# Optimization experiments

Measured on AMD Instinct MI355X. Metric: run time of the kernel, lower is better.

## Reference

```python
import jax, jax.numpy as jnp
import numpy as np

B, T, D = 1, 4096, 1024
H, KD, VD = 16, 64, 64
MIN_THETA, MAX_THETA = 1.0, 10000.0


def setup_inputs() -> dict:
    key = jax.random.key(0)
    k0, k1, k2 = jax.random.split(key, 3)
    x = jax.random.normal(k0, (B, T, D), dtype=jnp.float32)
    W_in = jax.random.normal(k1, ((2 * KD + VD) * H, D), dtype=jnp.float32) * 0.02
    b_in = jnp.zeros(((2 * KD + VD) * H,), dtype=jnp.float32)
    W_out = jax.random.normal(k2, (D, H * VD), dtype=jnp.float32) * 0.02
    b_out = jnp.zeros((D,), dtype=jnp.float32)
    return {"x": x, "W_in": W_in, "b_in": b_in, "W_out": W_out, "b_out": b_out}


def _sin_cos(t, d, dtype):
    # geometric sequence of thetas over half the head dim
    half = d // 2
    p = jnp.arange(half, dtype=dtype) / (half - 1)
    thetas = MIN_THETA * (MAX_THETA / MIN_THETA) ** p  # [half]
    pos = jnp.arange(t, dtype=dtype)[:, None] / thetas[None, :]  # [T, half]
    return jnp.sin(pos), jnp.cos(pos)


def _rope(x, sin, cos):
    d = x.shape[-1] // 2
    x_hi, x_lo = x[..., :d], x[..., d:]
    y_lo = x_lo * cos + x_hi * sin
    y_hi = x_hi * cos - x_lo * sin
    return jnp.concatenate([y_lo, y_hi], axis=-1)


def reference(x, W_in, b_in, W_out, b_out):
    b, t, _ = x.shape
    proj = x @ W_in.T + b_in  # [B, T, (2KD+VD)*H]
    i1, i2 = KD * H, 2 * KD * H
    q = proj[..., :i1].reshape(b, t, H, KD).transpose(0, 2, 1, 3)   # [B,H,T,KD]
    k = proj[..., i1:i2].reshape(b, t, H, KD).transpose(0, 2, 1, 3)
    v = proj[..., i2:].reshape(b, t, H, VD).transpose(0, 2, 1, 3)   # [B,H,T,VD]
    sin, cos = _sin_cos(t, KD, x.dtype)
    q = _rope(q, sin, cos)
    k = _rope(k, sin, cos)
    scale = 1.0 / np.sqrt(KD)
    att = jnp.einsum('bhqd,bhkd->bhqk', q, k) * jnp.asarray(scale, x.dtype)
    mask = jnp.tril(jnp.ones((t, t), dtype=bool))  # causal
    att = jnp.where(mask[None, None], att, jnp.asarray(-jnp.inf, x.dtype))
    att = jax.nn.softmax(att, axis=-1)
    y = jnp.einsum('bhqk,bhkd->bhqd', att, v)
    y = y.transpose(0, 2, 1, 3).reshape(b, t, H * VD)
    return y @ W_out.T + b_out
```

## Files before the change

kernel.cpp:

```cpp
#include <hip/hip_runtime.h>
#include <math.h>

#define T_SEQ 4096
#define DMODEL 1024
#define NH 16
#define HD 64
#define NQT (T_SEQ / 64)

typedef _Float16 f16x4 __attribute__((ext_vector_type(4)));
typedef _Float16 f16x8 __attribute__((ext_vector_type(8)));
typedef float f32x4 __attribute__((ext_vector_type(4)));

#define HTD ((size_t)NH * T_SEQ * HD)

__global__ __launch_bounds__(256)
void sincos_table_kernel(float* __restrict__ tab) {
    int idx = blockIdx.x * 256 + threadIdx.x;
    if (idx >= T_SEQ * 32) return;
    int t = idx >> 5, j = idx & 31;
    double p = (double)((float)j / 31.0f);
    float theta = (float)pow(10000.0, p);
    float ang = (float)t / theta;
    double a = (double)ang;
    tab[t * 64 + j]      = (float)sin(a);
    tab[t * 64 + 32 + j] = (float)cos(a);
}

__global__ __launch_bounds__(256)
void cast3_kernel(const float* __restrict__ x, const float* __restrict__ wi,
                  const float* __restrict__ wo, _Float16* __restrict__ x16,
                  _Float16* __restrict__ wi16, _Float16* __restrict__ wo16) {
    size_t gid = (size_t)blockIdx.x * 256 + threadIdx.x;
    const float* src; _Float16* dst; size_t i;
    if (gid < 524288)       { src = x;  dst = x16;  i = gid; }
    else if (gid < 917504)  { src = wi; dst = wi16; i = gid - 524288; }
    else                    { src = wo; dst = wo16; i = gid - 917504; }
    float4 a = *((const float4*)src + i * 2);
    float4 b = *((const float4*)src + i * 2 + 1);
    f16x8 o = {(_Float16)a.x, (_Float16)a.y, (_Float16)a.z, (_Float16)a.w,
               (_Float16)b.x, (_Float16)b.y, (_Float16)b.z, (_Float16)b.w};
    *((f16x8*)dst + i) = o;
}

__global__ __launch_bounds__(256)
void rope16_kernel(_Float16* __restrict__ q16, _Float16* __restrict__ k16,
                   const float* __restrict__ tab) {
    int idx = blockIdx.x * 256 + threadIdx.x;
    int j = idx & 31;
    int t = (idx >> 5) & (T_SEQ - 1);
    int h = (idx >> 17) & (NH - 1);
    int z = idx >> 21;
    float s = tab[t * 64 + j];
    float c = tab[t * 64 + 32 + j];
    _Float16* base = (z ? k16 : q16) + ((size_t)h * T_SEQ + t) * HD;
    float a = (float)base[j], b = (float)base[j + 32];
    float lo = b * c + a * s;
    float hi = a * c - b * s;
    if (z == 0) { lo *= 0.125f; hi *= 0.125f; }
    base[j]      = (_Float16)lo;
    base[j + 32] = (_Float16)hi;
}

template<int EPI>
__global__ __launch_bounds__(256)
void gemm16_kernel(const _Float16* __restrict__ A, const _Float16* __restrict__ B,
                   const float* __restrict__ bias, float* __restrict__ out,
                   _Float16* __restrict__ outv, int M, int N, int K, int gx) {
    __shared__ _Float16 Alds[128 * 64];
    __shared__ _Float16 Blds[128 * 64];
    const int tid = threadIdx.x;
    const int w = tid >> 6, lane = tid & 63, lq = lane & 15, lg = lane >> 4;
    const int wr = w >> 1, wc = w & 1;

    int cpx = (int)gridDim.x >> 3;
    int tileid = (blockIdx.x & 7) * cpx + (blockIdx.x >> 3);
    const int bx = tileid % gx, by = tileid / gx;
    const int row0 = by * 128, col0 = bx * 128;

    const int ra = tid >> 1, ha = tid & 1;
    const _Float16* Ap = A + (size_t)(row0 + ra) * K + ha * 32;
    const _Float16* Bp = B + (size_t)(col0 + ra) * K + ha * 32;
    char* Awr = (char*)Alds + ra * 128;
    char* Bwr = (char*)Blds + ra * 128;
    int wsw[4];
#pragma unroll
    for (int j = 0; j < 4; ++j) wsw[j] = ((ha * 4 + j) ^ (ra & 7)) * 16;

    f32x4 acc[4][4] = {};
    f16x8 sa[4], sb[4];
#pragma unroll
    for (int j = 0; j < 4; ++j) {
        sa[j] = *(const f16x8*)(Ap + j * 8);
        sb[j] = *(const f16x8*)(Bp + j * 8);
    }

    const int nkt = K >> 6;
    for (int kt = 0; kt < nkt; ++kt) {
        __syncthreads();
#pragma unroll
        for (int j = 0; j < 4; ++j) {
            *(f16x8*)(Awr + wsw[j]) = sa[j];
            *(f16x8*)(Bwr + wsw[j]) = sb[j];
        }
        __syncthreads();
        if (kt + 1 < nkt) {
            int kn = (kt + 1) << 6;
#pragma unroll
            for (int j = 0; j < 4; ++j) {
                sa[j] = *(const f16x8*)(Ap + kn + j * 8);
                sb[j] = *(const f16x8*)(Bp + kn + j * 8);
            }
        }
#pragma unroll
        for (int ks = 0; ks < 2; ++ks) {
            f16x8 af[4], bf[4];
            const int cofs = ((ks * 4 + lg) ^ (lq & 7)) * 16;
#pragma unroll
            for (int i = 0; i < 4; ++i) {
                int rA = wr * 64 + i * 16 + lq;
                int rB = wc * 64 + i * 16 + lq;
                af[i] = *(const f16x8*)((char*)Alds + rA * 128 + cofs);
                bf[i] = *(const f16x8*)((char*)Blds + rB * 128 + cofs);
            }
#pragma unroll
            for (int mi = 0; mi < 4; ++mi)
#pragma unroll
                for (int nj = 0; nj < 4; ++nj)
                    acc[mi][nj] = __builtin_amdgcn_mfma_f32_16x16x32_f16(
                        af[mi], bf[nj], acc[mi][nj], 0, 0, 0);
        }
    }

    if (EPI == 0) {
#pragma unroll
        for (int nj = 0; nj < 4; ++nj) {
            int n = col0 + wc * 64 + nj * 16 + lq;
            float bv = bias[n];
#pragma unroll
            for (int mi = 0; mi < 4; ++mi) {
                int t0 = row0 + wr * 64 + mi * 16 + lg * 4;
#pragma unroll
                for (int r = 0; r < 4; ++r)
                    out[(size_t)(t0 + r) * N + n] = acc[mi][nj][r] + bv;
            }
        }
    } else {
        const int tensor = col0 >> 10;
        const int m0b = row0 + wr * 64;
        if (tensor == 2) {
#pragma unroll
            for (int nj = 0; nj < 4; ++nj) {
                int n = col0 + wc * 64 + nj * 16 + lq;
                int nn = n & 1023; int hh = nn >> 6, d = nn & 63;
                float bv = bias[n];
                _Float16* dv = outv + 2 * HTD + (size_t)(hh * 64 + d) * T_SEQ;
#pragma unroll
                for (int mi = 0; mi < 4; ++mi) {
                    int t0 = m0b + mi * 16 + lg * 4;
                    f16x4 val = {(_Float16)(acc[mi][nj][0] + bv),
                                 (_Float16)(acc[mi][nj][1] + bv),
                                 (_Float16)(acc[mi][nj][2] + bv),
                                 (_Float16)(acc[mi][nj][3] + bv)};
                    *(f16x4*)(dv + t0) = val;
                }
            }
        } else {
            _Float16* dst = outv + (size_t)tensor * HTD;
#pragma unroll
            for (int nj = 0; nj < 4; ++nj) {
                int n = col0 + wc * 64 + nj * 16 + lq;
                int nn = n & 1023; int hh = nn >> 6, d = nn & 63;
                float bv = bias[n];
                _Float16* dcol = dst + (size_t)hh * T_SEQ * HD + d;
#pragma unroll
                for (int mi = 0; mi < 4; ++mi) {
                    int t0 = m0b + mi * 16 + lg * 4;
#pragma unroll
                    for (int r = 0; r < 4; ++r)
                        dcol[(size_t)(t0 + r) * HD] = (_Float16)(acc[mi][nj][r] + bv);
                }
            }
        }
    }
}

__global__ __launch_bounds__(256)
void attn_kernel(const _Float16* __restrict__ q16, const _Float16* __restrict__ k16,
                 const _Float16* __restrict__ v16t, _Float16* __restrict__ y16) {
    __shared__ _Float16 Klds[2][64 * 64];
    __shared__ _Float16 Vlds[2][64 * 64];
    __shared__ _Float16 Plds[4 * 16 * 64];

    const int tid  = threadIdx.x;
    const int w    = tid >> 6;
    const int lane = tid & 63;
    const int lq   = lane & 15;
    const int lg   = lane >> 4;

    const int bid  = blockIdx.x;
    const int h    = ((bid & 7) << 1) | ((bid >> 3) & 1);
    const int pr   = bid >> 4;

    const _Float16* qh = q16  + (size_t)h * T_SEQ * HD;
    const _Float16* kh = k16  + (size_t)h * T_SEQ * HD;
    const _Float16* vh = v16t + (size_t)h * HD * T_SEQ;

    const int srow = tid >> 4;
    const int scol = (tid & 15) * 4;
    const int schk = (tid & 15) >> 1;
    const int ssub = (tid & 1) * 8;

    _Float16* Pw = Plds + w * 1024;

    for (int half = 0; half < 2; ++half) {
        const int qt = half ? pr : (NQT - 1 - pr);
        const int q0 = qt * 64;
        const int qrow = q0 + w * 16 + lq;

        f16x8 qf[2];
        qf[0] = *(const f16x8*)(qh + (size_t)qrow * HD + lg * 8);
        qf[1] = *(const f16x8*)(qh + (size_t)qrow * HD + lg * 8 + 32);

        float m_r = -3e38f, l_r = 0.f;
        f32x4 acco[4] = {};

        f16x4 kreg[4], vreg[4];
#pragma unroll
        for (int it = 0; it < 4; ++it) {
            int row = srow + it * 16;
            kreg[it] = *(const f16x4*)(kh + (size_t)row * HD + scol);
            vreg[it] = *(const f16x4*)(vh + (size_t)row * T_SEQ + scol);
        }
        __syncthreads();
#pragma unroll
        for (int it = 0; it < 4; ++it) {
            int row = srow + it * 16;
            int chunk = schk ^ (row & 7);
            *(f16x4*)((char*)Klds[0] + row * 128 + chunk * 16 + ssub) = kreg[it];
            *(f16x4*)((char*)Vlds[0] + row * 128 + chunk * 16 + ssub) = vreg[it];
        }

        int cur = 0;
        for (int kt = 0; kt <= qt; ++kt) {
            __syncthreads();
            if (kt < qt) {
                const int k0n = (kt + 1) * 64;
#pragma unroll
                for (int it = 0; it < 4; ++it) {
                    int row = srow + it * 16;
                    kreg[it] = *(const f16x4*)(kh + (size_t)(k0n + row) * HD + scol);
                    vreg[it] = *(const f16x4*)(vh + (size_t)row * T_SEQ + k0n + scol);
                }
            }

            f32x4 s[4] = {};
            __builtin_amdgcn_s_setprio(1);
#pragma unroll
            for (int mb = 0; mb < 4; ++mb) {
                int row = mb * 16 + lq;
#pragma unroll
                for (int ks = 0; ks < 2; ++ks) {
                    f16x8 kf = *(const f16x8*)((char*)Klds[cur] + row * 128 +
                                               (((lg + 4 * ks) ^ (lq & 7)) * 16));
                    s[mb] = __builtin_amdgcn_mfma_f32_16x16x32_f16(kf, qf[ks], s[mb], 0, 0, 0);
                }
            }
            __builtin_amdgcn_s_setprio(0);
            if (kt == qt) {
                const int qloc = w * 16 + lq;
#pragma unroll
                for (int mb = 0; mb < 4; ++mb)
#pragma unroll
                    for (int r = 0; r < 4; ++r)
                        if (mb * 16 + lg * 4 + r > qloc) s[mb][r] = -3e38f;
            }

            float tmax = s[0][0];
#pragma unroll
            for (int mb = 0; mb < 4; ++mb)
#pragma unroll
                for (int r = 0; r < 4; ++r) tmax = fmaxf(tmax, s[mb][r]);
            tmax = fmaxf(tmax, __shfl_xor(tmax, 16));
            tmax = fmaxf(tmax, __shfl_xor(tmax, 32));
            if (__ballot(tmax > m_r + 8.0f)) {
                float mn  = fmaxf(m_r, tmax);
                float scl = __expf(m_r - mn);
                m_r = mn;
                l_r *= scl;
#pragma unroll
                for (int mb = 0; mb < 4; ++mb)
#pragma unroll
                    for (int r = 0; r < 4; ++r) acco[mb][r] *= scl;
            }

            float tsum = 0.f;
#pragma unroll
            for (int mb = 0; mb < 4; ++mb) {
                float p0 = __expf(s[mb][0] - m_r), p1 = __expf(s[mb][1] - m_r);
                float p2 = __expf(s[mb][2] - m_r), p3 = __expf(s[mb][3] - m_r);
                tsum += (p0 + p1) + (p2 + p3);
                f16x4 pk = {(_Float16)p0, (_Float16)p1, (_Float16)p2, (_Float16)p3};
                *(f16x4*)(Pw + (mb * 2 + (lg >> 1)) * 128 + lq * 8 + (lg & 1) * 4) = pk;
            }
            tsum += __shfl_xor(tsum, 16);
            tsum += __shfl_xor(tsum, 32);
            l_r += tsum;

            f16x8 pf[2];
#pragma unroll
            for (int ks = 0; ks < 2; ++ks)
                pf[ks] = *(const f16x8*)(Pw + (lg + 4 * ks) * 128 + lq * 8);
            __builtin_amdgcn_s_setprio(1);
#pragma unroll
            for (int mb = 0; mb < 4; ++mb) {
                int row = mb * 16 + lq;
#pragma unroll
                for (int ks = 0; ks < 2; ++ks) {
                    f16x8 vf = *(const f16x8*)((char*)Vlds[cur] + row * 128 +
                                               (((lg + 4 * ks) ^ (lq & 7)) * 16));
                    acco[mb] = __builtin_amdgcn_mfma_f32_16x16x32_f16(vf, pf[ks], acco[mb], 0, 0, 0);
                }
            }
            __builtin_amdgcn_s_setprio(0);

            if (kt < qt) {
#pragma unroll
                for (int it = 0; it < 4; ++it) {
                    int row = srow + it * 16;
                    int chunk = schk ^ (row & 7);
                    *(f16x4*)((char*)Klds[cur ^ 1] + row * 128 + chunk * 16 + ssub) = kreg[it];
                    *(f16x4*)((char*)Vlds[cur ^ 1] + row * 128 + chunk * 16 + ssub) = vreg[it];
                }
                cur ^= 1;
            }
        }

        float inv = 1.f / l_r;
#pragma unroll
        for (int mb = 0; mb < 4; ++mb) {
            f16x4 o = {(_Float16)(acco[mb][0] * inv), (_Float16)(acco[mb][1] * inv),
                       (_Float16)(acco[mb][2] * inv), (_Float16)(acco[mb][3] * inv)};
            *(f16x4*)(y16 + (size_t)qrow * DMODEL + h * HD + mb * 16 + lg * 4) = o;
        }
    }
}

extern "C" void kernel_launch(void* const* d_in, const int* in_sizes, int n_in,
                              void* d_out, int out_size, void* d_ws, size_t ws_size,
                              hipStream_t stream) {
    const float* x     = (const float*)d_in[0];
    const float* W_in  = (const float*)d_in[1];
    const float* b_in  = (const float*)d_in[2];
    const float* W_out = (const float*)d_in[3];
    const float* b_out = (const float*)d_in[4];
    float* out = (float*)d_out;

    float* ws = (float*)d_ws;
    float* tab = ws;
    _Float16* fb   = (_Float16*)(ws + (size_t)T_SEQ * 64);
    _Float16* q16  = fb;
    _Float16* k16  = fb + HTD;
    _Float16* v16t = fb + 2 * HTD;
    _Float16* x16  = fb + 3 * HTD;
    _Float16* y16  = x16;
    _Float16* wi16 = x16 + (size_t)T_SEQ * DMODEL;
    _Float16* wo16 = wi16 + (size_t)3072 * DMODEL;

    sincos_table_kernel<<<(T_SEQ * 32 + 255) / 256, 256, 0, stream>>>(tab);
    cast3_kernel<<<4096, 256, 0, stream>>>(x, W_in, W_out, x16, wi16, wo16);

    gemm16_kernel<1><<<768, 256, 0, stream>>>(
        x16, wi16, b_in, nullptr, q16, T_SEQ, 3072, DMODEL, 24);

    rope16_kernel<<<(2 * NH * T_SEQ * 32) / 256, 256, 0, stream>>>(q16, k16, tab);

    attn_kernel<<<512, 256, 0, stream>>>(q16, k16, v16t, y16);

    gemm16_kernel<0><<<256, 256, 0, stream>>>(
        y16, wo16, b_out, out, nullptr, T_SEQ, DMODEL, DMODEL, 8);
}
```

Before: 237.1 us.

## Process two query tiles per block sharing each K/V tile; use exp2 softmax

The attention kernel now gives each block a 128-row query tile, split into two 64-row halves that share every loaded K/V LDS tile. Previously each block handled two 64-row tiles one after the other, loading K/V separately for each. This halves K/V global and LDS traffic per query row. The softmax folds log2(e) into the Q scale so it can use exp2f, and it defers the cross-lane row-sum reduction to the end. The price is more registers for two accumulator sets, a larger P buffer in LDS, and less even causal load balancing across blocks.

```diff
diff --git a/kernel.cpp b/kernel.cpp
--- a/kernel.cpp
+++ b/kernel.cpp
@@ -56,7 +56,7 @@
     float a = (float)base[j], b = (float)base[j + 32];
     float lo = b * c + a * s;
     float hi = a * c - b * s;
-    if (z == 0) { lo *= 0.125f; hi *= 0.125f; }
+    if (z == 0) { lo *= 0.18033688f; hi *= 0.18033688f; }
     base[j]      = (_Float16)lo;
     base[j + 32] = (_Float16)hi;
 }
@@ -184,12 +184,44 @@
     }
 }
 
+__device__ __forceinline__ void softmax_step(f32x4 s[4], float& m, float& lp,
+                                             f32x4 acc[4], _Float16* Pw,
+                                             int lq, int lg) {
+    float tmax = s[0][0];
+#pragma unroll
+    for (int mb = 0; mb < 4; ++mb)
+#pragma unroll
+        for (int r = 0; r < 4; ++r) tmax = fmaxf(tmax, s[mb][r]);
+    if (__ballot(tmax > m + 11.5f)) {
+        float g = fmaxf(tmax, __shfl_xor(tmax, 16));
+        g = fmaxf(g, __shfl_xor(g, 32));
+        float mn  = fmaxf(m, g);
+        float scl = exp2f(m - mn);
+        m = mn;
+        lp *= scl;
+#pragma unroll
+        for (int mb = 0; mb < 4; ++mb)
+#pragma unroll
+            for (int r = 0; r < 4; ++r) acc[mb][r] *= scl;
+    }
+    float tsum = 0.f;
+#pragma unroll
+    for (int mb = 0; mb < 4; ++mb) {
+        float p0 = exp2f(s[mb][0] - m), p1 = exp2f(s[mb][1] - m);
+        float p2 = exp2f(s[mb][2] - m), p3 = exp2f(s[mb][3] - m);
+        tsum += (p0 + p1) + (p2 + p3);
+        f16x4 pk = {(_Float16)p0, (_Float16)p1, (_Float16)p2, (_Float16)p3};
+        *(f16x4*)(Pw + (mb * 2 + (lg >> 1)) * 128 + lq * 8 + (lg & 1) * 4) = pk;
+    }
+    lp += tsum;
+}
+
 __global__ __launch_bounds__(256)
 void attn_kernel(const _Float16* __restrict__ q16, const _Float16* __restrict__ k16,
                  const _Float16* __restrict__ v16t, _Float16* __restrict__ y16) {
     __shared__ _Float16 Klds[2][64 * 64];
     __shared__ _Float16 Vlds[2][64 * 64];
-    __shared__ _Float16 Plds[4 * 16 * 64];
+    __shared__ _Float16 Plds[8 * 16 * 64];
 
     const int tid  = threadIdx.x;
     const int w    = tid >> 6;
@@ -197,151 +229,145 @@
     const int lq   = lane & 15;
     const int lg   = lane >> 4;
 
-    const int bid  = blockIdx.x;
-    const int h    = ((bid & 7) << 1) | ((bid >> 3) & 1);
-    const int pr   = bid >> 4;
+    const int bid = blockIdx.x;
+    const int h   = ((bid & 7) << 1) | ((bid >> 3) & 1);
+    const int qt  = 31 - (bid >> 4);
+    const int q0  = qt * 128;
 
     const _Float16* qh = q16  + (size_t)h * T_SEQ * HD;
     const _Float16* kh = k16  + (size_t)h * T_SEQ * HD;
     const _Float16* vh = v16t + (size_t)h * HD * T_SEQ;
+
+    const int qrow0 = q0 + w * 16 + lq;
+    const int qrow1 = qrow0 + 64;
+
+    f16x8 qf0[2], qf1[2];
+    qf0[0] = *(const f16x8*)(qh + (size_t)qrow0 * HD + lg * 8);
+    qf0[1] = *(const f16x8*)(qh + (size_t)qrow0 * HD + lg * 8 + 32);
+    qf1[0] = *(const f16x8*)(qh + (size_t)qrow1 * HD + lg * 8);
+    qf1[1] = *(const f16x8*)(qh + (size_t)qrow1 * HD + lg * 8 + 32);
 
     const int srow = tid >> 4;
     const int scol = (tid & 15) * 4;
     const int schk = (tid & 15) >> 1;
     const int ssub = (tid & 1) * 8;
 
-    _Float16* Pw = Plds + w * 1024;
-
-    for (int half = 0; half < 2; ++half) {
-        const int qt = half ? pr : (NQT - 1 - pr);
-        const int q0 = qt * 64;
-        const int qrow = q0 + w * 16 + lq;
-
-        f16x8 qf[2];
-        qf[0] = *(const f16x8*)(qh + (size_t)qrow * HD + lg * 8);
-        qf[1] = *(const f16x8*)(qh + (size_t)qrow * HD + lg * 8 + 32);
-
-        float m_r = -3e38f, l_r = 0.f;
-        f32x4 acco[4] = {};
-
-        f16x4 kreg[4], vreg[4];
-#pragma unroll
-        for (int it = 0; it < 4; ++it) {
-            int row = srow + it * 16;
-            kreg[it] = *(const f16x4*)(kh + (size_t)row * HD + scol);
-            vreg[it] = *(const f16x4*)(vh + (size_t)row * T_SEQ + scol);
-        }
+    _Float16* Pw0 = Plds + (w * 2 + 0) * 1024;
+    _Float16* Pw1 = Plds + (w * 2 + 1) * 1024;
+
+    float m0 = -3e38f, m1 = -3e38f, lp0 = 0.f, lp1 = 0.f;
+    f32x4 acc0[4] = {}, acc1[4] = {};
+
+    const int ktmax  = 2 * qt + 1;
+    const int kt0max = 2 * qt;
+
+    f16x4 kreg[4], vreg[4];
+#pragma unroll
+    for (int it = 0; it < 4; ++it) {
+        int row = srow + it * 16;
+        kreg[it] = *(const f16x4*)(kh + (size_t)row * HD + scol);
+        vreg[it] = *(const f16x4*)(vh + (size_t)row * T_SEQ + scol);
+    }
+#pragma unroll
+    for (int it = 0; it < 4; ++it) {
+        int row = srow + it * 16;
+        int chunk = schk ^ (row & 7);
+        *(f16x4*)((char*)Klds[0] + row * 128 + chunk * 16 + ssub) = kreg[it];
+        *(f16x4*)((char*)Vlds[0] + row * 128 + chunk * 16 + ssub) = vreg[it];
+    }
+
+    int cur = 0;
+    for (int kt = 0; kt <= ktmax; ++kt) {
         __syncthreads();
-#pragma unroll
-        for (int it = 0; it < 4; ++it) {
-            int row = srow + it * 16;
-            int chunk = schk ^ (row & 7);
-            *(f16x4*)((char*)Klds[0] + row * 128 + chunk * 16 + ssub) = kreg[it];
-            *(f16x4*)((char*)Vlds[0] + row * 128 + chunk * 16 + ssub) = vreg[it];
-        }
-
-        int cur = 0;
-        for (int kt = 0; kt <= qt; ++kt) {
-            __syncthreads();
-            if (kt < qt) {
-                const int k0n = (kt + 1) * 64;
-#pragma unroll
-                for (int it = 0; it < 4; ++it) {
-                    int row = srow + it * 16;
-                    kreg[it] = *(const f16x4*)(kh + (size_t)(k0n + row) * HD + scol);
-                    vreg[it] = *(const f16x4*)(vh + (size_t)row * T_SEQ + k0n + scol);
-                }
-            }
-
-            f32x4 s[4] = {};
-            __builtin_amdgcn_s_setprio(1);
-#pragma unroll
-            for (int mb = 0; mb < 4; ++mb) {
-                int row = mb * 16 + lq;
-#pragma unroll
-                for (int ks = 0; ks < 2; ++ks) {
-                    f16x8 kf = *(const f16x8*)((char*)Klds[cur] + row * 128 +
-                                               (((lg + 4 * ks) ^ (lq & 7)) * 16));
-                    s[mb] = __builtin_amdgcn_mfma_f32_16x16x32_f16(kf, qf[ks], s[mb], 0, 0, 0);
-                }
-            }
-            __builtin_amdgcn_s_setprio(0);
-            if (kt == qt) {
-                const int qloc = w * 16 + lq;
-#pragma unroll
-                for (int mb = 0; mb < 4; ++mb)
-#pragma unroll
-                    for (int r = 0; r < 4; ++r)
-                        if (mb * 16 + lg * 4 + r > qloc) s[mb][r] = -3e38f;
-            }
-
-            float tmax = s[0][0];
+        if (kt < ktmax) {
+            const int k0n = (kt + 1) * 64;
+#pragma unroll
+            for (int it = 0; it < 4; ++it) {
+                int row = srow + it * 16;
+                kreg[it] = *(const f16x4*)(kh + (size_t)(k0n + row) * HD + scol);
+                vreg[it] = *(const f16x4*)(vh + (size_t)row * T_SEQ + k0n + scol);
+            }
+        }
+        const bool a0 = (kt <= kt0max);
+
+        f32x4 s0[4] = {}, s1[4] = {};
+        __builtin_amdgcn_s_setprio(1);
+#pragma unroll
+        for (int mb = 0; mb < 4; ++mb) {
+            int row = mb * 16 + lq;
+#pragma unroll
+            for (int ks = 0; ks < 2; ++ks) {
+                f16x8 kf = *(const f16x8*)((char*)Klds[cur] + row * 128 +
+                                           (((lg + 4 * ks) ^ (lq & 7)) * 16));
+                if (a0) s0[mb] = __builtin_amdgcn_mfma_f32_16x16x32_f16(kf, qf0[ks], s0[mb], 0, 0, 0);
+                s1[mb] = __builtin_amdgcn_mfma_f32_16x16x32_f16(kf, qf1[ks], s1[mb], 0, 0, 0);
+            }
+        }
+        __builtin_amdgcn_s_setprio(0);
+
+        const int qloc = w * 16 + lq;
+        if (kt == kt0max) {
 #pragma unroll
             for (int mb = 0; mb < 4; ++mb)
 #pragma unroll
-                for (int r = 0; r < 4; ++r) tmax = fmaxf(tmax, s[mb][r]);
-            tmax = fmaxf(tmax, __shfl_xor(tmax, 16));
-            tmax = fmaxf(tmax, __shfl_xor(tmax, 32));
-            if (__ballot(tmax > m_r + 8.0f)) {
-                float mn  = fmaxf(m_r, tmax);
-                float scl = __expf(m_r - mn);
-                m_r = mn;
-                l_r *= scl;
-#pragma unroll
-                for (int mb = 0; mb < 4; ++mb)
-#pragma unroll
-                    for (int r = 0; r < 4; ++r) acco[mb][r] *= scl;
-            }
-
-            float tsum = 0.f;
-#pragma unroll
-            for (int mb = 0; mb < 4; ++mb) {
-                float p0 = __expf(s[mb][0] - m_r), p1 = __expf(s[mb][1] - m_r);
-                float p2 = __expf(s[mb][2] - m_r), p3 = __expf(s[mb][3] - m_r);
-                tsum += (p0 + p1) + (p2 + p3);
-                f16x4 pk = {(_Float16)p0, (_Float16)p1, (_Float16)p2, (_Float16)p3};
-                *(f16x4*)(Pw + (mb * 2 + (lg >> 1)) * 128 + lq * 8 + (lg & 1) * 4) = pk;
-            }
-            tsum += __shfl_xor(tsum, 16);
-            tsum += __shfl_xor(tsum, 32);
-            l_r += tsum;
-
-            f16x8 pf[2];
-#pragma unroll
-            for (int ks = 0; ks < 2; ++ks)
-                pf[ks] = *(const f16x8*)(Pw + (lg + 4 * ks) * 128 + lq * 8);
-            __builtin_amdgcn_s_setprio(1);
-#pragma unroll
-            for (int mb = 0; mb < 4; ++mb) {
-                int row = mb * 16 + lq;
-#pragma unroll
-                for (int ks = 0; ks < 2; ++ks) {
-                    f16x8 vf = *(const f16x8*)((char*)Vlds[cur] + row * 128 +
-                                               (((lg + 4 * ks) ^ (lq & 7)) * 16));
-                    acco[mb] = __builtin_amdgcn_mfma_f32_16x16x32_f16(vf, pf[ks], acco[mb], 0, 0, 0);
-                }
-            }
-            __builtin_amdgcn_s_setprio(0);
-
-            if (kt < qt) {
-#pragma unroll
-                for (int it = 0; it < 4; ++it) {
-                    int row = srow + it * 16;
-                    int chunk = schk ^ (row & 7);
-                    *(f16x4*)((char*)Klds[cur ^ 1] + row * 128 + chunk * 16 + ssub) = kreg[it];
-                    *(f16x4*)((char*)Vlds[cur ^ 1] + row * 128 + chunk * 16 + ssub) = vreg[it];
-                }
-                cur ^= 1;
-            }
-        }
-
-        float inv = 1.f / l_r;
+                for (int r = 0; r < 4; ++r)
+                    if (mb * 16 + lg * 4 + r > qloc) s0[mb][r] = -3e38f;
+        }
+        if (kt == ktmax) {
+#pragma unroll
+            for (int mb = 0; mb < 4; ++mb)
+#pragma unroll
+                for (int r = 0; r < 4; ++r)
+                    if (mb * 16 + lg * 4 + r > qloc) s1[mb][r] = -3e38f;
+        }
+
+        if (a0) softmax_step(s0, m0, lp0, acc0, Pw0, lq, lg);
+        softmax_step(s1, m1, lp1, acc1, Pw1, lq, lg);
+
+        f16x8 pf0[2], pf1[2];
+        if (a0) {
+            pf0[0] = *(const f16x8*)(Pw0 + lg * 128 + lq * 8);
+            pf0[1] = *(const f16x8*)(Pw0 + (lg + 4) * 128 + lq * 8);
+        }
+        pf1[0] = *(const f16x8*)(Pw1 + lg * 128 + lq * 8);
+        pf1[1] = *(const f16x8*)(Pw1 + (lg + 4) * 128 + lq * 8);
+        __builtin_amdgcn_s_setprio(1);
 #pragma unroll
         for (int mb = 0; mb < 4; ++mb) {
-            f16x4 o = {(_Float16)(acco[mb][0] * inv), (_Float16)(acco[mb][1] * inv),
-                       (_Float16)(acco[mb][2] * inv), (_Float16)(acco[mb][3] * inv)};
-            *(f16x4*)(y16 + (size_t)qrow * DMODEL + h * HD + mb * 16 + lg * 4) = o;
-        }
+            int row = mb * 16 + lq;
+#pragma unroll
+            for (int ks = 0; ks < 2; ++ks) {
+                f16x8 vf = *(const f16x8*)((char*)Vlds[cur] + row * 128 +
+                                           (((lg + 4 * ks) ^ (lq & 7)) * 16));
+                if (a0) acc0[mb] = __builtin_amdgcn_mfma_f32_16x16x32_f16(vf, pf0[ks], acc0[mb], 0, 0, 0);
+                acc1[mb] = __builtin_amdgcn_mfma_f32_16x16x32_f16(vf, pf1[ks], acc1[mb], 0, 0, 0);
+            }
+        }
+        __builtin_amdgcn_s_setprio(0);
+
+        if (kt < ktmax) {
+#pragma unroll
+            for (int it = 0; it < 4; ++it) {
+                int row = srow + it * 16;
+                int chunk = schk ^ (row & 7);
+                *(f16x4*)((char*)Klds[cur ^ 1] + row * 128 + chunk * 16 + ssub) = kreg[it];
+                *(f16x4*)((char*)Vlds[cur ^ 1] + row * 128 + chunk * 16 + ssub) = vreg[it];
+            }
+            cur ^= 1;
+        }
+    }
+
+    float ls0 = lp0 + __shfl_xor(lp0, 16); ls0 += __shfl_xor(ls0, 32);
+    float ls1 = lp1 + __shfl_xor(lp1, 16); ls1 += __shfl_xor(ls1, 32);
+    float inv0 = 1.f / ls0, inv1 = 1.f / ls1;
+#pragma unroll
+    for (int mb = 0; mb < 4; ++mb) {
+        f16x4 o0 = {(_Float16)(acc0[mb][0] * inv0), (_Float16)(acc0[mb][1] * inv0),
+                    (_Float16)(acc0[mb][2] * inv0), (_Float16)(acc0[mb][3] * inv0)};
+        *(f16x4*)(y16 + (size_t)qrow0 * DMODEL + h * HD + mb * 16 + lg * 4) = o0;
+        f16x4 o1 = {(_Float16)(acc1[mb][0] * inv1), (_Float16)(acc1[mb][1] * inv1),
+                    (_Float16)(acc1[mb][2] * inv1), (_Float16)(acc1[mb][3] * inv1)};
+        *(f16x4*)(y16 + (size_t)qrow1 * DMODEL + h * HD + mb * 16 + lg * 4) = o1;
     }
 }
 
```

Result: slower. 318.1 us (+34.2%).

## Split attention KV range into two chunks with separate combine kernel

Applied to the files above, without the earlier changes.

The attention kernel no longer pairs a long and a short query tile per block. Each query tile's causal key range is split into two halves handled by separate blocks (2048 blocks instead of 512), and each writes fp32 partial outputs with its running max and sum to a workspace. A new combine kernel merges the two partials and writes the fp16 output. The softmax also switches to exp2 with log2(e) folded into the Q scale, and the row-sum reduction is deferred to the end. This adds parallelism and balances load, at the cost of an extra launch and fp32 partial-buffer traffic.

```diff
diff --git a/kernel.cpp b/kernel.cpp
--- a/kernel.cpp
+++ b/kernel.cpp
@@ -12,6 +12,7 @@
 typedef float f32x4 __attribute__((ext_vector_type(4)));
 
 #define HTD ((size_t)NH * T_SEQ * HD)
+#define PREC 68
 
 __global__ __launch_bounds__(256)
 void sincos_table_kernel(float* __restrict__ tab) {
@@ -56,7 +57,7 @@
     float a = (float)base[j], b = (float)base[j + 32];
     float lo = b * c + a * s;
     float hi = a * c - b * s;
-    if (z == 0) { lo *= 0.125f; hi *= 0.125f; }
+    if (z == 0) { lo *= 0.18033688f; hi *= 0.18033688f; }
     base[j]      = (_Float16)lo;
     base[j + 32] = (_Float16)hi;
 }
@@ -184,9 +185,41 @@
     }
 }
 
+__device__ __forceinline__ void softmax_step(f32x4 s[4], float& m, float& lp,
+                                             f32x4 acc[4], _Float16* Pw,
+                                             int lq, int lg) {
+    float tmax = s[0][0];
+#pragma unroll
+    for (int mb = 0; mb < 4; ++mb)
+#pragma unroll
+        for (int r = 0; r < 4; ++r) tmax = fmaxf(tmax, s[mb][r]);
+    if (__ballot(tmax > m + 11.5f)) {
+        float g = fmaxf(tmax, __shfl_xor(tmax, 16));
+        g = fmaxf(g, __shfl_xor(g, 32));
+        float mn  = fmaxf(m, g);
+        float scl = exp2f(m - mn);
+        m = mn;
+        lp *= scl;
+#pragma unroll
+        for (int mb = 0; mb < 4; ++mb)
+#pragma unroll
+            for (int r = 0; r < 4; ++r) acc[mb][r] *= scl;
+    }
+    float tsum = 0.f;
+#pragma unroll
+    for (int mb = 0; mb < 4; ++mb) {
+        float p0 = exp2f(s[mb][0] - m), p1 = exp2f(s[mb][1] - m);
+        float p2 = exp2f(s[mb][2] - m), p3 = exp2f(s[mb][3] - m);
+        tsum += (p0 + p1) + (p2 + p3);
+        f16x4 pk = {(_Float16)p0, (_Float16)p1, (_Float16)p2, (_Float16)p3};
+        *(f16x4*)(Pw + (mb * 2 + (lg >> 1)) * 128 + lq * 8 + (lg & 1) * 4) = pk;
+    }
+    lp += tsum;
+}
+
 __global__ __launch_bounds__(256)
 void attn_kernel(const _Float16* __restrict__ q16, const _Float16* __restrict__ k16,
-                 const _Float16* __restrict__ v16t, _Float16* __restrict__ y16) {
+                 const _Float16* __restrict__ v16t, float* __restrict__ part) {
     __shared__ _Float16 Klds[2][64 * 64];
     __shared__ _Float16 Vlds[2][64 * 64];
     __shared__ _Float16 Plds[4 * 16 * 64];
@@ -197,13 +230,25 @@
     const int lq   = lane & 15;
     const int lg   = lane >> 4;
 
-    const int bid  = blockIdx.x;
-    const int h    = ((bid & 7) << 1) | ((bid >> 3) & 1);
-    const int pr   = bid >> 4;
+    const int bid   = blockIdx.x;
+    const int h     = ((bid & 7) << 1) | ((bid >> 3) & 1);
+    const int rest  = bid >> 4;
+    const int qt    = (NQT - 1) - (rest >> 1);
+    const int chunk = rest & 1;
+    const int nkt   = qt + 1;
+    const int half0 = (nkt + 1) >> 1;
+    const int c0    = chunk ? half0 : 0;
+    const int c1    = chunk ? nkt   : half0;
 
     const _Float16* qh = q16  + (size_t)h * T_SEQ * HD;
     const _Float16* kh = k16  + (size_t)h * T_SEQ * HD;
     const _Float16* vh = v16t + (size_t)h * HD * T_SEQ;
+
+    const int qrow = qt * 64 + w * 16 + lq;
+
+    f16x8 qf[2];
+    qf[0] = *(const f16x8*)(qh + (size_t)qrow * HD + lg * 8);
+    qf[1] = *(const f16x8*)(qh + (size_t)qrow * HD + lg * 8 + 32);
 
     const int srow = tid >> 4;
     const int scol = (tid & 15) * 4;
@@ -212,38 +257,29 @@
 
     _Float16* Pw = Plds + w * 1024;
 
-    for (int half = 0; half < 2; ++half) {
-        const int qt = half ? pr : (NQT - 1 - pr);
-        const int q0 = qt * 64;
-        const int qrow = q0 + w * 16 + lq;
-
-        f16x8 qf[2];
-        qf[0] = *(const f16x8*)(qh + (size_t)qrow * HD + lg * 8);
-        qf[1] = *(const f16x8*)(qh + (size_t)qrow * HD + lg * 8 + 32);
-
-        float m_r = -3e38f, l_r = 0.f;
-        f32x4 acco[4] = {};
-
+    float m_r = -3e38f, lp = 0.f;
+    f32x4 acc[4] = {};
+
+    if (c0 < c1) {
         f16x4 kreg[4], vreg[4];
 #pragma unroll
         for (int it = 0; it < 4; ++it) {
             int row = srow + it * 16;
-            kreg[it] = *(const f16x4*)(kh + (size_t)row * HD + scol);
-            vreg[it] = *(const f16x4*)(vh + (size_t)row * T_SEQ + scol);
-        }
-        __syncthreads();
+            kreg[it] = *(const f16x4*)(kh + (size_t)(c0 * 64 + row) * HD + scol);
+            vreg[it] = *(const f16x4*)(vh + (size_t)row * T_SEQ + c0 * 64 + scol);
+        }
 #pragma unroll
         for (int it = 0; it < 4; ++it) {
             int row = srow + it * 16;
-            int chunk = schk ^ (row & 7);
-            *(f16x4*)((char*)Klds[0] + row * 128 + chunk * 16 + ssub) = kreg[it];
-            *(f16x4*)((char*)Vlds[0] + row * 128 + chunk * 16 + ssub) = vreg[it];
+            int chk = schk ^ (row & 7);
+            *(f16x4*)((char*)Klds[0] + row * 128 + chk * 16 + ssub) = kreg[it];
+            *(f16x4*)((char*)Vlds[0] + row * 128 + chk * 16 + ssub) = vreg[it];
         }
 
         int cur = 0;
-        for (int kt = 0; kt <= qt; ++kt) {
+        for (int kt = c0; kt < c1; ++kt) {
             __syncthreads();
-            if (kt < qt) {
+            if (kt + 1 < c1) {
                 const int k0n = (kt + 1) * 64;
 #pragma unroll
                 for (int it = 0; it < 4; ++it) {
@@ -275,41 +311,11 @@
                         if (mb * 16 + lg * 4 + r > qloc) s[mb][r] = -3e38f;
             }
 
-            float tmax = s[0][0];
-#pragma unroll
-            for (int mb = 0; mb < 4; ++mb)
-#pragma unroll
-                for (int r = 0; r < 4; ++r) tmax = fmaxf(tmax, s[mb][r]);
-            tmax = fmaxf(tmax, __shfl_xor(tmax, 16));
-            tmax = fmaxf(tmax, __shfl_xor(tmax, 32));
-            if (__ballot(tmax > m_r + 8.0f)) {
-                float mn  = fmaxf(m_r, tmax);
-                float scl = __expf(m_r - mn);
-                m_r = mn;
-                l_r *= scl;
-#pragma unroll
-                for (int mb = 0; mb < 4; ++mb)
-#pragma unroll
-                    for (int r = 0; r < 4; ++r) acco[mb][r] *= scl;
-            }
-
-            float tsum = 0.f;
-#pragma unroll
-            for (int mb = 0; mb < 4; ++mb) {
-                float p0 = __expf(s[mb][0] - m_r), p1 = __expf(s[mb][1] - m_r);
-                float p2 = __expf(s[mb][2] - m_r), p3 = __expf(s[mb][3] - m_r);
-                tsum += (p0 + p1) + (p2 + p3);
-                f16x4 pk = {(_Float16)p0, (_Float16)p1, (_Float16)p2, (_Float16)p3};
-                *(f16x4*)(Pw + (mb * 2 + (lg >> 1)) * 128 + lq * 8 + (lg & 1) * 4) = pk;
-            }
-            tsum += __shfl_xor(tsum, 16);
-            tsum += __shfl_xor(tsum, 32);
-            l_r += tsum;
+            softmax_step(s, m_r, lp, acc, Pw, lq, lg);
 
             f16x8 pf[2];
-#pragma unroll
-            for (int ks = 0; ks < 2; ++ks)
-                pf[ks] = *(const f16x8*)(Pw + (lg + 4 * ks) * 128 + lq * 8);
+            pf[0] = *(const f16x8*)(Pw + lg * 128 + lq * 8);
+            pf[1] = *(const f16x8*)(Pw + (lg + 4) * 128 + lq * 8);
             __builtin_amdgcn_s_setprio(1);
 #pragma unroll
             for (int mb = 0; mb < 4; ++mb) {
@@ -318,30 +324,62 @@
                 for (int ks = 0; ks < 2; ++ks) {
                     f16x8 vf = *(const f16x8*)((char*)Vlds[cur] + row * 128 +
                                                (((lg + 4 * ks) ^ (lq & 7)) * 16));
-                    acco[mb] = __builtin_amdgcn_mfma_f32_16x16x32_f16(vf, pf[ks], acco[mb], 0, 0, 0);
+                    acc[mb] = __builtin_amdgcn_mfma_f32_16x16x32_f16(vf, pf[ks], acc[mb], 0, 0, 0);
                 }
             }
             __builtin_amdgcn_s_setprio(0);
 
-            if (kt < qt) {
+            if (kt + 1 < c1) {
 #pragma unroll
                 for (int it = 0; it < 4; ++it) {
                     int row = srow + it * 16;
-                    int chunk = schk ^ (row & 7);
-                    *(f16x4*)((char*)Klds[cur ^ 1] + row * 128 + chunk * 16 + ssub) = kreg[it];
-                    *(f16x4*)((char*)Vlds[cur ^ 1] + row * 128 + chunk * 16 + ssub) = vreg[it];
+                    int chk = schk ^ (row & 7);
+                    *(f16x4*)((char*)Klds[cur ^ 1] + row * 128 + chk * 16 + ssub) = kreg[it];
+                    *(f16x4*)((char*)Vlds[cur ^ 1] + row * 128 + chk * 16 + ssub) = vreg[it];
                 }
                 cur ^= 1;
             }
         }
-
-        float inv = 1.f / l_r;
-#pragma unroll
-        for (int mb = 0; mb < 4; ++mb) {
-            f16x4 o = {(_Float16)(acco[mb][0] * inv), (_Float16)(acco[mb][1] * inv),
-                       (_Float16)(acco[mb][2] * inv), (_Float16)(acco[mb][3] * inv)};
-            *(f16x4*)(y16 + (size_t)qrow * DMODEL + h * HD + mb * 16 + lg * 4) = o;
-        }
+    }
+
+    float lsum = lp + __shfl_xor(lp, 16); lsum += __shfl_xor(lsum, 32);
+    float* rec = part + ((size_t)((h * NQT + qt) * 2 + chunk) * 64 + w * 16 + lq) * PREC;
+#pragma unroll
+    for (int mb = 0; mb < 4; ++mb)
+        *(float4*)(rec + mb * 16 + lg * 4) =
+            make_float4(acc[mb][0], acc[mb][1], acc[mb][2], acc[mb][3]);
+    if (lg == 0) { rec[64] = m_r; rec[65] = lsum; }
+}
+
+__global__ __launch_bounds__(256)
+void combine_kernel(const float* __restrict__ part, _Float16* __restrict__ y16) {
+    const int bid = blockIdx.x;
+    const int h = bid >> 6, qt = bid & 63;
+    const int r  = threadIdx.x >> 2;
+    const int dq = (threadIdx.x & 3) * 16;
+
+    const float* r0 = part + ((size_t)((h * NQT + qt) * 2 + 0) * 64 + r) * PREC;
+    const float* r1 = part + ((size_t)((h * NQT + qt) * 2 + 1) * 64 + r) * PREC;
+    float m0 = r0[64], l0 = r0[65];
+    float m1 = r1[64], l1 = r1[65];
+    float mx = fmaxf(m0, m1);
+    float w0 = exp2f(m0 - mx), w1 = exp2f(m1 - mx);
+    float inv = 1.f / (l0 * w0 + l1 * w1);
+    w0 *= inv; w1 *= inv;
+
+    const int qrow = qt * 64 + r;
+    _Float16* yp = y16 + (size_t)qrow * DMODEL + h * HD + dq;
+#pragma unroll
+    for (int j = 0; j < 2; ++j) {
+        float4 a0 = *(const float4*)(r0 + dq + j * 8);
+        float4 b0 = *(const float4*)(r0 + dq + j * 8 + 4);
+        float4 a1 = *(const float4*)(r1 + dq + j * 8);
+        float4 b1 = *(const float4*)(r1 + dq + j * 8 + 4);
+        f16x8 o = {(_Float16)(a0.x * w0 + a1.x * w1), (_Float16)(a0.y * w0 + a1.y * w1),
+                   (_Float16)(a0.z * w0 + a1.z * w1), (_Float16)(a0.w * w0 + a1.w * w1),
+                   (_Float16)(b0.x * w0 + b1.x * w1), (_Float16)(b0.y * w0 + b1.y * w1),
+                   (_Float16)(b0.z * w0 + b1.z * w1), (_Float16)(b0.w * w0 + b1.w * w1)};
+        *(f16x8*)(yp + j * 8) = o;
     }
 }
 
@@ -365,6 +403,7 @@
     _Float16* y16  = x16;
     _Float16* wi16 = x16 + (size_t)T_SEQ * DMODEL;
     _Float16* wo16 = wi16 + (size_t)3072 * DMODEL;
+    float* part = (float*)(wo16 + (size_t)DMODEL * DMODEL);
 
     sincos_table_kernel<<<(T_SEQ * 32 + 255) / 256, 256, 0, stream>>>(tab);
     cast3_kernel<<<4096, 256, 0, stream>>>(x, W_in, W_out, x16, wi16, wo16);
@@ -374,7 +413,9 @@
 
     rope16_kernel<<<(2 * NH * T_SEQ * 32) / 256, 256, 0, stream>>>(q16, k16, tab);
 
-    attn_kernel<<<512, 256, 0, stream>>>(q16, k16, v16t, y16);
+    attn_kernel<<<2048, 256, 0, stream>>>(q16, k16, v16t, part);
+
+    combine_kernel<<<NH * NQT, 256, 0, stream>>>(part, y16);
 
     gemm16_kernel<0><<<256, 256, 0, stream>>>(
         y16, wo16, b_out, out, nullptr, T_SEQ, DMODEL, DMODEL, 8);
```

New measurement: 233.3 us. Within noise of the previous version (-1.6%).
